# Kernel optimization log

Measured on AMD Instinct MI355X. Metric: run time of the kernel, lower is better.

The kernel has to match this reference:

```python
import jax, jax.numpy as jnp
import numpy as np

H_DIM = 768
N_HEADS = 12
SEQ = 4096
MLP_RATIO = 4
EPS = 1e-5


def layernorm(x, g, b):
    mu = jnp.mean(x, axis=-1, keepdims=True)
    var = jnp.var(x, axis=-1, keepdims=True)
    return (x - mu) * jax.lax.rsqrt(var + EPS) * g + b


def setup_inputs() -> dict:
    key = jax.random.key(0)
    ks = jax.random.split(key, 16)
    C, F = H_DIM, MLP_RATIO * H_DIM
    s = 1.0 / np.sqrt(C)
    inp = {
        "x": jax.random.normal(ks[0], (1, SEQ, C), dtype=jnp.float32),
        "Wq": jax.random.normal(ks[1], (C, C), dtype=jnp.float32) * s,
        "bq": jnp.zeros((C,), jnp.float32),
        "Wk": jax.random.normal(ks[2], (C, C), dtype=jnp.float32) * s,
        "bk": jnp.zeros((C,), jnp.float32),
        "Wv": jax.random.normal(ks[3], (C, C), dtype=jnp.float32) * s,
        "bv": jnp.zeros((C,), jnp.float32),
        "Wo": jax.random.normal(ks[4], (C, C), dtype=jnp.float32) * s,
        "bo": jnp.zeros((C,), jnp.float32),
        "ln1_g": jnp.ones((C,), jnp.float32),
        "ln1_b": jnp.zeros((C,), jnp.float32),
        "W1": jax.random.normal(ks[5], (C, F), dtype=jnp.float32) * s,
        "b1": jnp.zeros((F,), jnp.float32),
        "W2": jax.random.normal(ks[6], (F, C), dtype=jnp.float32) * (1.0 / np.sqrt(F)),
        "b2": jnp.zeros((C,), jnp.float32),
        "ln2_g": jnp.ones((C,), jnp.float32),
        "ln2_b": jnp.zeros((C,), jnp.float32),
    }
    return inp


def reference(x, Wq, bq, Wk, bk, Wv, bv, Wo, bo, ln1_g, ln1_b, W1, b1, W2, b2, ln2_g, ln2_b):
    B, T, C = x.shape
    N, D = N_HEADS, C // N_HEADS

    # --- masked self-attention (naive, materializes T x T scores) ---
    q = (x @ Wq + bq).reshape(B, T, N, D).transpose(0, 2, 1, 3)  # [B,N,T,D]
    k = (x @ Wk + bk).reshape(B, T, N, D).transpose(0, 2, 1, 3)
    v = (x @ Wv + bv).reshape(B, T, N, D).transpose(0, 2, 1, 3)

    logits = jnp.einsum("bntd,bnsd->bnts", q, k) / jnp.sqrt(jnp.float32(D))
    causal = jnp.tril(jnp.ones((T, T), dtype=bool))  # True where allowed
    logits = jnp.where(causal, logits, -jnp.inf)
    attn = jax.nn.softmax(logits, axis=-1)
    out = jnp.einsum("bnts,bnsd->bntd", attn, v)
    out = out.transpose(0, 2, 1, 3).reshape(B, T, C)
    attn_out = out @ Wo + bo

    # --- post-norm residual + MLP ---
    h = layernorm(x + attn_out, ln1_g, ln1_b)
    mlp = jax.nn.gelu(h @ W1 + b1, approximate=False) @ W2 + b2
    y = layernorm(h + mlp, ln2_g, ln2_b)
    return y
```

## Files before the change

kernel.cpp:

```cpp
#include <hip/hip_runtime.h>
#include <hip/hip_bf16.h>
#include <math.h>

#define T_SEQ 4096
#define C_DIM 768
#define N_HEADS 12
#define D_HEAD 64
#define F_DIM 3072
#define EPS 1e-5f
#define QSCALE 0.18033688011112042f

typedef __attribute__((ext_vector_type(8))) short short8;
typedef __attribute__((ext_vector_type(4))) float f32x4;

__device__ __forceinline__ void gload_lds16(const void* g, void* lds) {
    __builtin_amdgcn_global_load_lds(
        (const __attribute__((address_space(1))) unsigned int*)g,
        (__attribute__((address_space(3))) unsigned int*)lds, 16, 0, 0);
}

__launch_bounds__(256)
__global__ void transpose_w4(const float* __restrict__ Wq, const float* __restrict__ Wk,
                             const float* __restrict__ Wv, const float* __restrict__ Wo,
                             __hip_bfloat16* __restrict__ Wqkv_t,
                             __hip_bfloat16* __restrict__ Wo_t) {
    __shared__ float tile[64][65];
    const int z = blockIdx.z;
    const float* W = (z == 0) ? Wq : (z == 1) ? Wk : (z == 2) ? Wv : Wo;
    __hip_bfloat16* Wt = (z < 3) ? (Wqkv_t + (size_t)z * C_DIM * C_DIM) : Wo_t;
    const int k0 = blockIdx.x * 64;
    const int n0 = blockIdx.y * 64;
    const int tid = threadIdx.x;
    const int c = tid & 63;
    const int r0 = (tid >> 6) * 16;
    #pragma unroll
    for (int i = 0; i < 16; ++i)
        tile[r0 + i][c] = W[(size_t)(k0 + r0 + i) * C_DIM + n0 + c];
    __syncthreads();
    #pragma unroll
    for (int i = 0; i < 16; ++i)
        Wt[(size_t)(n0 + r0 + i) * C_DIM + k0 + c] = __float2bfloat16(tile[c][r0 + i]);
}

__launch_bounds__(256)
__global__ void transpose_w(const float* __restrict__ W, __hip_bfloat16* __restrict__ Wt,
                            int K, int N) {
    __shared__ float tile[64][65];
    const int k0 = blockIdx.x * 64;
    const int n0 = blockIdx.y * 64;
    const int tid = threadIdx.x;
    const int c = tid & 63;
    const int r0 = (tid >> 6) * 16;
    #pragma unroll
    for (int i = 0; i < 16; ++i)
        tile[r0 + i][c] = W[(size_t)(k0 + r0 + i) * N + n0 + c];
    __syncthreads();
    #pragma unroll
    for (int i = 0; i < 16; ++i)
        Wt[(size_t)(n0 + r0 + i) * K + k0 + c] = __float2bfloat16(tile[c][r0 + i]);
}

__launch_bounds__(256)
__global__ void concat_bias(const float* __restrict__ bq, const float* __restrict__ bk,
                            const float* __restrict__ bv, float* __restrict__ o) {
    const int i = blockIdx.x * 256 + threadIdx.x;
    if (i < C_DIM) {
        o[i] = bq[i];
        o[C_DIM + i] = bk[i];
        o[2 * C_DIM + i] = bv[i];
    }
}

__launch_bounds__(256)
__global__ void f32_to_bf16_vec(const float* __restrict__ in, __hip_bfloat16* __restrict__ out,
                                int n4) {
    const int i = blockIdx.x * 256 + threadIdx.x;
    if (i < n4) {
        const float4 v = *reinterpret_cast<const float4*>(&in[(size_t)i * 4]);
        ushort4 u;
        u.x = __bfloat16_as_ushort(__float2bfloat16(v.x));
        u.y = __bfloat16_as_ushort(__float2bfloat16(v.y));
        u.z = __bfloat16_as_ushort(__float2bfloat16(v.z));
        u.w = __bfloat16_as_ushort(__float2bfloat16(v.w));
        *reinterpret_cast<ushort4*>(&out[(size_t)i * 4]) = u;
    }
}

#define GBM 128
#define GBN 128
#define GBK 64

template<int MODE>
__launch_bounds__(256)
__global__ void gemm_mfma(const __hip_bfloat16* __restrict__ A,
                          const __hip_bfloat16* __restrict__ Bt,
                          const float* __restrict__ bias,
                          float* __restrict__ outf,
                          __hip_bfloat16* __restrict__ outq,
                          __hip_bfloat16* __restrict__ outk,
                          __hip_bfloat16* __restrict__ outvt,
                          int M, int N, int K) {
    __shared__ __hip_bfloat16 As[2][GBM][GBK];
    __shared__ __hip_bfloat16 Bs[2][GBN][GBK];

    const int tid = threadIdx.x;
    const int l   = tid & 63;
    const int w   = tid >> 6;
    const int lr  = l & 15;
    const int lg  = l >> 4;
    const int wr  = w >> 1;
    const int wc  = w & 1;
    const int bm  = blockIdx.y * GBM;
    const int bn  = blockIdx.x * GBN;

    const int srow  = l >> 3;
    const int skoff = (l & 7) * 8;

    f32x4 acc[4][4];
    #pragma unroll
    for (int m = 0; m < 4; ++m)
        #pragma unroll
        for (int n = 0; n < 4; ++n)
            acc[m][n] = {0.f, 0.f, 0.f, 0.f};

    auto stage = [&](int buf, int k0) {
        #pragma unroll
        for (int i = 0; i < 4; ++i) {
            const int rb = (w * 4 + i) * 8;
            gload_lds16(&A[(size_t)(bm + rb + srow) * K + k0 + skoff], &As[buf][rb][0]);
            gload_lds16(&Bt[(size_t)(bn + rb + srow) * K + k0 + skoff], &Bs[buf][rb][0]);
        }
    };

    const int nk = K / GBK;
    stage(0, 0);
    for (int kt = 0; kt < nk; ++kt) {
        const int cur = kt & 1;
        __syncthreads();
        if (kt + 1 < nk) stage(cur ^ 1, (kt + 1) * GBK);

        #pragma unroll
        for (int kk = 0; kk < 2; ++kk) {
            short8 af[4], bf[4];
            #pragma unroll
            for (int m = 0; m < 4; ++m)
                af[m] = *reinterpret_cast<const short8*>(
                    &As[cur][wr * 64 + m * 16 + lr][kk * 32 + lg * 8]);
            #pragma unroll
            for (int n = 0; n < 4; ++n)
                bf[n] = *reinterpret_cast<const short8*>(
                    &Bs[cur][wc * 64 + n * 16 + lr][kk * 32 + lg * 8]);
            #pragma unroll
            for (int m = 0; m < 4; ++m)
                #pragma unroll
                for (int n = 0; n < 4; ++n)
                    acc[m][n] = __builtin_amdgcn_mfma_f32_16x16x32_bf16(af[m], bf[n], acc[m][n], 0, 0, 0);
        }
    }

    #pragma unroll
    for (int m = 0; m < 4; ++m) {
        #pragma unroll
        for (int rr = 0; rr < 4; ++rr) {
            const int row = bm + wr * 64 + m * 16 + lg * 4 + rr;
            #pragma unroll
            for (int n = 0; n < 4; ++n) {
                const int col = bn + wc * 64 + n * 16 + lr;
                float v = acc[m][n][rr] + bias[col];
                if constexpr (MODE == 0) {
                    outf[(size_t)row * N + col] = v;
                } else if constexpr (MODE == 1) {
                    v = 0.5f * v * (1.0f + erff(v * 0.70710678118654752f));
                    outq[(size_t)row * N + col] = __float2bfloat16(v);
                } else {
                    if (col < C_DIM)
                        outq[(size_t)row * C_DIM + col] = __float2bfloat16(v * QSCALE);
                    else if (col < 2 * C_DIM)
                        outk[(size_t)row * C_DIM + (col - C_DIM)] = __float2bfloat16(v);
                    else
                        outvt[(size_t)(col - 2 * C_DIM) * T_SEQ + row] = __float2bfloat16(v);
                }
            }
        }
    }
}

#define QBLK 64
#define KVB 128

__launch_bounds__(256)
__global__ void attn_mfma(const __hip_bfloat16* __restrict__ q,
                          const __hip_bfloat16* __restrict__ k,
                          const __hip_bfloat16* __restrict__ vt,
                          __hip_bfloat16* __restrict__ o) {
    __shared__ __hip_bfloat16 Ks[2][KVB][64];
    __shared__ __hip_bfloat16 Vts[2][D_HEAD][KVB];
    __shared__ __hip_bfloat16 Ps[4][16][KVB];

    const int tid  = threadIdx.x;
    const int wid  = tid >> 6;
    const int lane = tid & 63;
    const int lr   = lane & 15;
    const int lg   = lane >> 4;

    const int h  = blockIdx.x;
    const int q0 = T_SEQ - QBLK - blockIdx.y * QBLK;
    const int qw = q0 + wid * 16;

    const int ksrc = 8 * ((lane & 7) ^ (lane >> 3));
    const int kr   = lane >> 3;
    const int vr   = lane >> 4;
    const int vs   = lane & 15;

    short8 aq[2];
    #pragma unroll
    for (int kk = 0; kk < 2; ++kk)
        aq[kk] = *reinterpret_cast<const short8*>(
            &q[(size_t)(qw + lr) * C_DIM + h * D_HEAD + kk * 32 + lg * 8]);

    f32x4 o_acc[4];
    #pragma unroll
    for (int dc = 0; dc < 4; ++dc) o_acc[dc] = {0.f, 0.f, 0.f, 0.f};
    float m_run[4], l_part[4];
    #pragma unroll
    for (int r = 0; r < 4; ++r) { m_run[r] = -1e30f; l_part[r] = 0.f; }

    auto stage = [&](int buf, int s0) {
        #pragma unroll
        for (int i = 0; i < 4; ++i) {
            const int rb = wid * 32 + i * 8;
            gload_lds16(&k[(size_t)(s0 + rb + kr) * C_DIM + h * D_HEAD + ksrc],
                        &Ks[buf][rb][0]);
        }
        #pragma unroll
        for (int i = 0; i < 4; ++i) {
            const int vb = wid * 16 + i * 4;
            const int vsrc = 8 * (vs ^ (i * 4 + vr));
            gload_lds16(&vt[(size_t)(h * D_HEAD + vb + vr) * T_SEQ + s0 + vsrc],
                        &Vts[buf][vb][0]);
        }
    };

    const int n_tiles = (q0 + QBLK + KVB - 1) / KVB;

    stage(0, 0);
    __syncthreads();

    for (int t = 0; t < n_tiles; ++t) {
        const int cur = t & 1;
        if (t + 1 < n_tiles) stage(cur ^ 1, (t + 1) * KVB);

        f32x4 s_acc[8];
        __builtin_amdgcn_s_setprio(1);
        #pragma unroll
        for (int c = 0; c < 8; ++c) {
            s_acc[c] = {0.f, 0.f, 0.f, 0.f};
            #pragma unroll
            for (int kk = 0; kk < 2; ++kk) {
                const short8 bk8 = *reinterpret_cast<const short8*>(
                    &Ks[cur][c * 16 + lr][8 * ((4 * kk + lg) ^ (lr & 7))]);
                s_acc[c] = __builtin_amdgcn_mfma_f32_16x16x32_bf16(aq[kk], bk8, s_acc[c], 0, 0, 0);
            }
        }
        __builtin_amdgcn_s_setprio(0);

        if (t == n_tiles - 1) {
            const int s0 = t * KVB;
            #pragma unroll
            for (int c = 0; c < 8; ++c)
                #pragma unroll
                for (int r = 0; r < 4; ++r) {
                    const int sg = s0 + c * 16 + lr;
                    const int qg = qw + lg * 4 + r;
                    if (sg > qg) s_acc[c][r] = -1e30f;
                }
        }

        float pm[4];
        #pragma unroll
        for (int r = 0; r < 4; ++r) {
            const float m0 = fmaxf(fmaxf(s_acc[0][r], s_acc[1][r]),
                                   fmaxf(s_acc[2][r], s_acc[3][r]));
            const float m1 = fmaxf(fmaxf(s_acc[4][r], s_acc[5][r]),
                                   fmaxf(s_acc[6][r], s_acc[7][r]));
            pm[r] = fmaxf(m0, m1);
        }
        const float need = fmaxf(fmaxf(pm[0] - m_run[0], pm[1] - m_run[1]),
                                 fmaxf(pm[2] - m_run[2], pm[3] - m_run[3]));
        if (!__all(need <= 8.0f)) {
            #pragma unroll
            for (int r = 0; r < 4; ++r) {
                float nm = pm[r];
                #pragma unroll
                for (int off = 1; off < 16; off <<= 1)
                    nm = fmaxf(nm, __shfl_xor(nm, off));
                nm = fmaxf(nm, m_run[r]);
                const float corr = __builtin_amdgcn_exp2f(m_run[r] - nm);
                m_run[r] = nm;
                l_part[r] *= corr;
                #pragma unroll
                for (int dc = 0; dc < 4; ++dc) o_acc[dc][r] *= corr;
            }
        }
        #pragma unroll
        for (int r = 0; r < 4; ++r) {
            const int qrow = lg * 4 + r;
            float ls = 0.f;
            #pragma unroll
            for (int c = 0; c < 8; ++c) {
                const float pv = __builtin_amdgcn_exp2f(s_acc[c][r] - m_run[r]);
                ls += pv;
                const int slot = (2 * c + (lr >> 3)) ^ qrow;
                Ps[wid][qrow][slot * 8 + (lr & 7)] = __float2bfloat16(pv);
            }
            l_part[r] += ls;
        }

        short8 ap[4];
        #pragma unroll
        for (int kk = 0; kk < 4; ++kk)
            ap[kk] = *reinterpret_cast<const short8*>(
                &Ps[wid][lr][8 * ((4 * kk + lg) ^ lr)]);
        __builtin_amdgcn_s_setprio(1);
        #pragma unroll
        for (int dc = 0; dc < 4; ++dc)
            #pragma unroll
            for (int kk = 0; kk < 4; ++kk) {
                const short8 bv8 = *reinterpret_cast<const short8*>(
                    &Vts[cur][dc * 16 + lr][8 * ((4 * kk + lg) ^ lr)]);
                o_acc[dc] = __builtin_amdgcn_mfma_f32_16x16x32_bf16(ap[kk], bv8, o_acc[dc], 0, 0, 0);
            }
        __builtin_amdgcn_s_setprio(0);

        __syncthreads();
    }

    #pragma unroll
    for (int r = 0; r < 4; ++r) {
        #pragma unroll
        for (int off = 1; off < 16; off <<= 1)
            l_part[r] += __shfl_xor(l_part[r], off);
    }

    #pragma unroll
    for (int dc = 0; dc < 4; ++dc)
        #pragma unroll
        for (int r = 0; r < 4; ++r)
            o[(size_t)(qw + lg * 4 + r) * C_DIM + h * D_HEAD + dc * 16 + lr] =
                __float2bfloat16(o_acc[dc][r] / l_part[r]);
}

template<bool WB16>
__launch_bounds__(256)
__global__ void add_ln(const float* __restrict__ a, const float* __restrict__ b,
                       const float* __restrict__ g, const float* __restrict__ beta,
                       float* __restrict__ outf, __hip_bfloat16* __restrict__ outb) {
    const int row = blockIdx.x;
    const int tid = threadIdx.x;
    const size_t rb = (size_t)row * C_DIM;

    float x[3];
    #pragma unroll
    for (int i = 0; i < 3; ++i) {
        const int c = tid + 256 * i;
        x[i] = a[rb + c] + b[rb + c];
    }

    float s = x[0] + x[1] + x[2];
    float s2 = x[0] * x[0] + x[1] * x[1] + x[2] * x[2];

    #pragma unroll
    for (int off = 32; off; off >>= 1) {
        s  += __shfl_xor(s, off);
        s2 += __shfl_xor(s2, off);
    }

    __shared__ float red[10];
    const int wave = tid >> 6;
    const int lane = tid & 63;
    if (lane == 0) { red[wave] = s; red[4 + wave] = s2; }
    __syncthreads();
    if (tid == 0) {
        const float ts  = red[0] + red[1] + red[2] + red[3];
        const float ts2 = red[4] + red[5] + red[6] + red[7];
        const float mu = ts * (1.0f / C_DIM);
        const float var = ts2 * (1.0f / C_DIM) - mu * mu;
        red[8] = mu;
        red[9] = rsqrtf(var + EPS);
    }
    __syncthreads();
    const float mu = red[8];
    const float rstd = red[9];

    #pragma unroll
    for (int i = 0; i < 3; ++i) {
        const int c = tid + 256 * i;
        const float v = (x[i] - mu) * rstd * g[c] + beta[c];
        outf[rb + c] = v;
        if constexpr (WB16) outb[rb + c] = __float2bfloat16(v);
    }
}

extern "C" void kernel_launch(void* const* d_in, const int* in_sizes, int n_in,
                              void* d_out, int out_size, void* d_ws, size_t ws_size,
                              hipStream_t stream) {
    const float* x     = (const float*)d_in[0];
    const float* Wq    = (const float*)d_in[1];
    const float* bq    = (const float*)d_in[2];
    const float* Wk    = (const float*)d_in[3];
    const float* bk    = (const float*)d_in[4];
    const float* Wv    = (const float*)d_in[5];
    const float* bv    = (const float*)d_in[6];
    const float* Wo    = (const float*)d_in[7];
    const float* bo    = (const float*)d_in[8];
    const float* ln1_g = (const float*)d_in[9];
    const float* ln1_b = (const float*)d_in[10];
    const float* W1    = (const float*)d_in[11];
    const float* b1    = (const float*)d_in[12];
    const float* W2    = (const float*)d_in[13];
    const float* b2    = (const float*)d_in[14];
    const float* ln2_g = (const float*)d_in[15];
    const float* ln2_b = (const float*)d_in[16];

    float* out = (float*)d_out;

    char* wsb = (char*)d_ws;
    const size_t TCb16 = (size_t)T_SEQ * C_DIM * 2;
    __hip_bfloat16* xb  = (__hip_bfloat16*)(wsb);
    __hip_bfloat16* qb  = (__hip_bfloat16*)(wsb + TCb16);
    __hip_bfloat16* kb  = (__hip_bfloat16*)(wsb + 2 * TCb16);
    __hip_bfloat16* vtb = (__hip_bfloat16*)(wsb + 3 * TCb16);
    __hip_bfloat16* mid = (__hip_bfloat16*)(wsb);
    float* proj = (float*)(wsb + 4 * TCb16);
    float* mlpo = proj;
    __hip_bfloat16* obuf = (__hip_bfloat16*)(wsb + 4 * TCb16 + 12582912);
    __hip_bfloat16* hb   = obuf;
    float* hbuf = (float*)(wsb + 4 * TCb16 + 12582912 + TCb16);
    char* we = wsb + 4 * TCb16 + 12582912 + TCb16 + 12582912;
    __hip_bfloat16* Wqkv_t = (__hip_bfloat16*)(we);
    __hip_bfloat16* Wo_t   = (__hip_bfloat16*)(we + 3538944);
    __hip_bfloat16* W1_t   = (__hip_bfloat16*)(we + 3538944 + 1179648);
    __hip_bfloat16* W2_t   = (__hip_bfloat16*)(we + 3538944 + 1179648 + 4718592);
    float* bqkv            = (float*)(we + 3538944 + 1179648 + 2 * 4718592);

    const dim3 blk256(256);

    transpose_w4<<<dim3(12, 12, 4), blk256, 0, stream>>>(Wq, Wk, Wv, Wo, Wqkv_t, Wo_t);
    transpose_w<<<dim3(12, 48), blk256, 0, stream>>>(W1, W1_t, C_DIM, F_DIM);
    transpose_w<<<dim3(48, 12), blk256, 0, stream>>>(W2, W2_t, F_DIM, C_DIM);
    concat_bias<<<dim3(3), blk256, 0, stream>>>(bq, bk, bv, bqkv);
    f32_to_bf16_vec<<<dim3(3072), blk256, 0, stream>>>(x, xb, T_SEQ * C_DIM / 4);

    gemm_mfma<2><<<dim3(3 * C_DIM / GBN, T_SEQ / GBM), blk256, 0, stream>>>(
        xb, Wqkv_t, bqkv, nullptr, qb, kb, vtb, T_SEQ, 3 * C_DIM, C_DIM);

    attn_mfma<<<dim3(N_HEADS, T_SEQ / QBLK), blk256, 0, stream>>>(qb, kb, vtb, obuf);

    gemm_mfma<0><<<dim3(C_DIM / GBN, T_SEQ / GBM), blk256, 0, stream>>>(
        obuf, Wo_t, bo, proj, nullptr, nullptr, nullptr, T_SEQ, C_DIM, C_DIM);

    add_ln<true><<<dim3(T_SEQ), blk256, 0, stream>>>(x, proj, ln1_g, ln1_b, hbuf, hb);

    gemm_mfma<1><<<dim3(F_DIM / GBN, T_SEQ / GBM), blk256, 0, stream>>>(
        hb, W1_t, b1, nullptr, mid, nullptr, nullptr, T_SEQ, F_DIM, C_DIM);

    gemm_mfma<0><<<dim3(C_DIM / GBN, T_SEQ / GBM), blk256, 0, stream>>>(
        mid, W2_t, b2, mlpo, nullptr, nullptr, nullptr, T_SEQ, C_DIM, F_DIM);

    add_ln<false><<<dim3(T_SEQ), blk256, 0, stream>>>(hbuf, mlpo, ln2_g, ln2_b, out, nullptr);
}
```

Measured before the change: 383.7 us.

## Template GEMM tile sizes, drop double buffering, transpose V separately

The GEMM kernel is templated on tile size, and the two C=768-output GEMMs (Wo and W2) now use 64x64 tiles so more blocks fill the CUs. The LDS double buffer is replaced by a single buffer that loads and then synchronizes each K step, which halves LDS use but removes the overlap of loads with MFMA work. The QKV GEMM now writes V row-major into a scratch buffer and a separate tiled transpose kernel produces V^T, replacing the strided scattered stores. This adds a kernel launch and an extra pass over V.

```diff
diff --git a/kernel.cpp b/kernel.cpp
--- a/kernel.cpp
+++ b/kernel.cpp
@@ -61,6 +61,24 @@
 }
 
 __launch_bounds__(256)
+__global__ void transpose_v(const __hip_bfloat16* __restrict__ V,
+                            __hip_bfloat16* __restrict__ Vt) {
+    __shared__ __hip_bfloat16 tile[64][65];
+    const int t0 = blockIdx.x * 64;
+    const int c0 = blockIdx.y * 64;
+    const int tid = threadIdx.x;
+    const int c = tid & 63;
+    const int r0 = (tid >> 6) * 16;
+    #pragma unroll
+    for (int i = 0; i < 16; ++i)
+        tile[r0 + i][c] = V[(size_t)(t0 + r0 + i) * C_DIM + c0 + c];
+    __syncthreads();
+    #pragma unroll
+    for (int i = 0; i < 16; ++i)
+        Vt[(size_t)(c0 + r0 + i) * T_SEQ + t0 + c] = tile[c][r0 + i];
+}
+
+__launch_bounds__(256)
 __global__ void concat_bias(const float* __restrict__ bq, const float* __restrict__ bk,
                             const float* __restrict__ bv, float* __restrict__ o) {
     const int i = blockIdx.x * 256 + threadIdx.x;
@@ -86,11 +104,9 @@
     }
 }
 
-#define GBM 128
-#define GBN 128
 #define GBK 64
 
-template<int MODE>
+template<int MODE, int TM, int TN>
 __launch_bounds__(256)
 __global__ void gemm_mfma(const __hip_bfloat16* __restrict__ A,
                           const __hip_bfloat16* __restrict__ Bt,
@@ -98,10 +114,14 @@
                           float* __restrict__ outf,
                           __hip_bfloat16* __restrict__ outq,
                           __hip_bfloat16* __restrict__ outk,
-                          __hip_bfloat16* __restrict__ outvt,
+                          __hip_bfloat16* __restrict__ outv,
                           int M, int N, int K) {
-    __shared__ __hip_bfloat16 As[2][GBM][GBK];
-    __shared__ __hip_bfloat16 Bs[2][GBN][GBK];
+    constexpr int WM = TM / 2, WN = TN / 2;
+    constexpr int FM = WM / 16, FN = WN / 16;
+    constexpr int AISS = TM / 32, BISS = TN / 32;
+
+    __shared__ __hip_bfloat16 As[TM][GBK];
+    __shared__ __hip_bfloat16 Bs[TN][GBK];
 
     const int tid = threadIdx.x;
     const int l   = tid & 63;
@@ -110,62 +130,60 @@
     const int lg  = l >> 4;
     const int wr  = w >> 1;
     const int wc  = w & 1;
-    const int bm  = blockIdx.y * GBM;
-    const int bn  = blockIdx.x * GBN;
+    const int bm  = blockIdx.y * TM;
+    const int bn  = blockIdx.x * TN;
 
     const int srow  = l >> 3;
     const int skoff = (l & 7) * 8;
 
-    f32x4 acc[4][4];
-    #pragma unroll
-    for (int m = 0; m < 4; ++m)
-        #pragma unroll
-        for (int n = 0; n < 4; ++n)
+    f32x4 acc[FM][FN];
+    #pragma unroll
+    for (int m = 0; m < FM; ++m)
+        #pragma unroll
+        for (int n = 0; n < FN; ++n)
             acc[m][n] = {0.f, 0.f, 0.f, 0.f};
 
-    auto stage = [&](int buf, int k0) {
-        #pragma unroll
-        for (int i = 0; i < 4; ++i) {
-            const int rb = (w * 4 + i) * 8;
-            gload_lds16(&A[(size_t)(bm + rb + srow) * K + k0 + skoff], &As[buf][rb][0]);
-            gload_lds16(&Bt[(size_t)(bn + rb + srow) * K + k0 + skoff], &Bs[buf][rb][0]);
-        }
-    };
-
-    const int nk = K / GBK;
-    stage(0, 0);
-    for (int kt = 0; kt < nk; ++kt) {
-        const int cur = kt & 1;
+    for (int k0 = 0; k0 < K; k0 += GBK) {
+        if (k0) __syncthreads();
+        #pragma unroll
+        for (int i = 0; i < AISS; ++i) {
+            const int rb = (w * AISS + i) * 8;
+            gload_lds16(&A[(size_t)(bm + rb + srow) * K + k0 + skoff], &As[rb][0]);
+        }
+        #pragma unroll
+        for (int i = 0; i < BISS; ++i) {
+            const int rb = (w * BISS + i) * 8;
+            gload_lds16(&Bt[(size_t)(bn + rb + srow) * K + k0 + skoff], &Bs[rb][0]);
+        }
         __syncthreads();
-        if (kt + 1 < nk) stage(cur ^ 1, (kt + 1) * GBK);
 
         #pragma unroll
         for (int kk = 0; kk < 2; ++kk) {
-            short8 af[4], bf[4];
-            #pragma unroll
-            for (int m = 0; m < 4; ++m)
+            short8 af[FM], bf[FN];
+            #pragma unroll
+            for (int m = 0; m < FM; ++m)
                 af[m] = *reinterpret_cast<const short8*>(
-                    &As[cur][wr * 64 + m * 16 + lr][kk * 32 + lg * 8]);
-            #pragma unroll
-            for (int n = 0; n < 4; ++n)
+                    &As[wr * WM + m * 16 + lr][kk * 32 + lg * 8]);
+            #pragma unroll
+            for (int n = 0; n < FN; ++n)
                 bf[n] = *reinterpret_cast<const short8*>(
-                    &Bs[cur][wc * 64 + n * 16 + lr][kk * 32 + lg * 8]);
-            #pragma unroll
-            for (int m = 0; m < 4; ++m)
+                    &Bs[wc * WN + n * 16 + lr][kk * 32 + lg * 8]);
+            #pragma unroll
+            for (int m = 0; m < FM; ++m)
                 #pragma unroll
-                for (int n = 0; n < 4; ++n)
+                for (int n = 0; n < FN; ++n)
                     acc[m][n] = __builtin_amdgcn_mfma_f32_16x16x32_bf16(af[m], bf[n], acc[m][n], 0, 0, 0);
         }
     }
 
     #pragma unroll
-    for (int m = 0; m < 4; ++m) {
+    for (int m = 0; m < FM; ++m) {
         #pragma unroll
         for (int rr = 0; rr < 4; ++rr) {
-            const int row = bm + wr * 64 + m * 16 + lg * 4 + rr;
-            #pragma unroll
-            for (int n = 0; n < 4; ++n) {
-                const int col = bn + wc * 64 + n * 16 + lr;
+            const int row = bm + wr * WM + m * 16 + lg * 4 + rr;
+            #pragma unroll
+            for (int n = 0; n < FN; ++n) {
+                const int col = bn + wc * WN + n * 16 + lr;
                 float v = acc[m][n][rr] + bias[col];
                 if constexpr (MODE == 0) {
                     outf[(size_t)row * N + col] = v;
@@ -178,7 +196,7 @@
                     else if (col < 2 * C_DIM)
                         outk[(size_t)row * C_DIM + (col - C_DIM)] = __float2bfloat16(v);
                     else
-                        outvt[(size_t)(col - 2 * C_DIM) * T_SEQ + row] = __float2bfloat16(v);
+                        outv[(size_t)row * C_DIM + (col - 2 * C_DIM)] = __float2bfloat16(v);
                 }
             }
         }
@@ -432,6 +450,7 @@
     __hip_bfloat16* vtb = (__hip_bfloat16*)(wsb + 3 * TCb16);
     __hip_bfloat16* mid = (__hip_bfloat16*)(wsb);
     float* proj = (float*)(wsb + 4 * TCb16);
+    __hip_bfloat16* vb = (__hip_bfloat16*)proj;
     float* mlpo = proj;
     __hip_bfloat16* obuf = (__hip_bfloat16*)(wsb + 4 * TCb16 + 12582912);
     __hip_bfloat16* hb   = obuf;
@@ -451,20 +470,22 @@
     concat_bias<<<dim3(3), blk256, 0, stream>>>(bq, bk, bv, bqkv);
     f32_to_bf16_vec<<<dim3(3072), blk256, 0, stream>>>(x, xb, T_SEQ * C_DIM / 4);
 
-    gemm_mfma<2><<<dim3(3 * C_DIM / GBN, T_SEQ / GBM), blk256, 0, stream>>>(
-        xb, Wqkv_t, bqkv, nullptr, qb, kb, vtb, T_SEQ, 3 * C_DIM, C_DIM);
+    gemm_mfma<2, 128, 128><<<dim3(3 * C_DIM / 128, T_SEQ / 128), blk256, 0, stream>>>(
+        xb, Wqkv_t, bqkv, nullptr, qb, kb, vb, T_SEQ, 3 * C_DIM, C_DIM);
+
+    transpose_v<<<dim3(T_SEQ / 64, C_DIM / 64), blk256, 0, stream>>>(vb, vtb);
 
     attn_mfma<<<dim3(N_HEADS, T_SEQ / QBLK), blk256, 0, stream>>>(qb, kb, vtb, obuf);
 
-    gemm_mfma<0><<<dim3(C_DIM / GBN, T_SEQ / GBM), blk256, 0, stream>>>(
+    gemm_mfma<0, 64, 64><<<dim3(C_DIM / 64, T_SEQ / 64), blk256, 0, stream>>>(
         obuf, Wo_t, bo, proj, nullptr, nullptr, nullptr, T_SEQ, C_DIM, C_DIM);
 
     add_ln<true><<<dim3(T_SEQ), blk256, 0, stream>>>(x, proj, ln1_g, ln1_b, hbuf, hb);
 
-    gemm_mfma<1><<<dim3(F_DIM / GBN, T_SEQ / GBM), blk256, 0, stream>>>(
+    gemm_mfma<1, 128, 128><<<dim3(F_DIM / 128, T_SEQ / 128), blk256, 0, stream>>>(
         hb, W1_t, b1, nullptr, mid, nullptr, nullptr, T_SEQ, F_DIM, C_DIM);
 
-    gemm_mfma<0><<<dim3(C_DIM / GBN, T_SEQ / GBM), blk256, 0, stream>>>(
+    gemm_mfma<0, 64, 64><<<dim3(C_DIM / 64, T_SEQ / 64), blk256, 0, stream>>>(
         mid, W2_t, b2, mlpo, nullptr, nullptr, nullptr, T_SEQ, C_DIM, F_DIM);
 
     add_ln<false><<<dim3(T_SEQ), blk256, 0, stream>>>(hbuf, mlpo, ln2_g, ln2_b, out, nullptr);
```

New measurement: 336.3 us. 1.14x faster.
